# Kernel optimization log

Hardware: AMD Instinct MI355X
Metric: run time of the kernel (lower is better)

The kernel has to match this reference:

```python
import jax, jax.numpy as jnp
import numpy as np

LEVEL = 20            # module default -> 21 max-pool passes, kernels 1x1 .. 41x41 (H,W only)
K_SIG = 10.0          # init arg k: sigmoid weight sharpness
N_POOL = LEVEL + 1    # len(max_pool)
DENOM = N_POOL + 1    # torch: level = len(max_pool) + 1 = 22


def _edge3d(mask):
    # Equivalent to F.conv3d(mask, filt, padding=1) > 0 where filt is the
    # in-plane Laplacian: center 1, 4 H/W-neighbors -0.25, zeros elsewhere.
    p = jnp.pad(mask, ((0, 0), (0, 0), (0, 0), (1, 1), (1, 1)))
    lap = mask - 0.25 * (p[..., :-2, 1:-1] + p[..., 2:, 1:-1]
                         + p[..., 1:-1, :-2] + p[..., 1:-1, 2:])
    return (lap > 0).astype(jnp.float32)


def _mp3(x):
    # stride-1 3x3 max pool over H,W with same padding (pads with -inf like torch MaxPool)
    return jax.lax.reduce_window(x, -jnp.inf, jax.lax.max,
                                 (1, 1, 1, 3, 3), (1, 1, 1, 1, 1),
                                 ((0, 0), (0, 0), (0, 0), (1, 1), (1, 1)))


def _cal_dist(mask):
    edge = _edge3d(mask)  # [B,1,D,H,W] binary
    # maxpool with window (2k+1)x(2k+1) on a binary map == k cascaded 3x3 dilations,
    # so sum_{k=0}^{LEVEL} maxpool_{2k+1}(edge) is computed incrementally.
    def body(i, carry):
        e, acc = carry
        return (_mp3(e), acc + e)
    _, acc = jax.lax.fori_loop(0, N_POOL, body, (edge, jnp.zeros_like(edge)))
    return (DENOM - acc) / DENOM


def setup_inputs() -> dict:
    key = jax.random.key(0)
    k1, k2 = jax.random.split(key)
    outputs = jax.random.uniform(k1, (2, 1, 64, 256, 256), dtype=jnp.float32)
    masks = jax.random.randint(k2, (2, 1, 64, 256, 256), 0, 2, dtype=jnp.int32)
    return {"outputs": outputs, "masks": masks}


def reference(outputs, masks):
    eps = 1e-6
    m = masks.astype(jnp.float32)
    dist = _cal_dist(m)
    weight = jax.lax.stop_gradient(2.0 / (1.0 + jnp.exp(K_SIG * dist)))
    b = outputs.shape[0]
    ow = (outputs.astype(jnp.float32) * weight).reshape(b, -1)
    mw = (m * weight).reshape(b, -1)
    intersect = jnp.sum(ow * m.reshape(b, -1), axis=1)
    input_area = jnp.sum(ow, axis=1)
    target_area = jnp.sum(mw, axis=1)
    batch_loss = 1.0 - 2.0 * intersect / (input_area + target_area + 2.0 * eps)
    batch_loss = jnp.where(target_area == 0, 0.0, batch_loss)
    return batch_loss.mean()
```

## Files before the change

### kernel.cpp

```cpp
#include <hip/hip_runtime.h>
#include <stdint.h>

typedef unsigned long long u64;

#define SLICES 128
#define WPS 1024
#define TOTAL_WORDS (SLICES * WPS)
#define NBLK3 512


__global__ __launch_bounds__(256) void k_pack(const int* __restrict__ masks,
                                              u64* __restrict__ mbits) {
    const int lane = threadIdx.x & 63;
    const int wave = (blockIdx.x * 256 + threadIdx.x) >> 6;
    const int nwaves = (gridDim.x * 256) >> 6;
    #pragma unroll 4
    for (int w = wave; w < TOTAL_WORDS; w += nwaves) {
        int v = masks[(size_t)w * 64 + lane];
        u64 bal = __ballot(v != 0);
        if (lane == 0) mbits[w] = bal;
    }
}

__global__ __launch_bounds__(256) void k_dilate(const u64* __restrict__ mbits,
                                                u64* __restrict__ planes) {
    __shared__ u64 rows[256][5];
    __shared__ u64 tmp[256][5];

    const int t = threadIdx.x;
    const int slice = blockIdx.x;
    const u64* mb = mbits + (size_t)slice * WPS;

    u64 m[4];
    #pragma unroll
    for (int j = 0; j < 4; ++j) { m[j] = mb[t * 4 + j]; rows[t][j] = m[j]; }
    __syncthreads();

    u64 c[4];
    {
        u64 up[4], dn[4];
        #pragma unroll
        for (int j = 0; j < 4; ++j) {
            up[j] = (t > 0)   ? rows[t - 1][j] : 0ull;
            dn[j] = (t < 255) ? rows[t + 1][j] : 0ull;
        }
        #pragma unroll
        for (int j = 0; j < 4; ++j) {
            u64 lf = (m[j] << 1) | (j > 0 ? (m[j - 1] >> 63) : 0ull);
            u64 rt = (m[j] >> 1) | (j < 3 ? (m[j + 1] << 63) : 0ull);
            c[j] = m[j] & ~(up[j] & dn[j] & lf & rt);
        }
    }

    u64 p[5][4];
    #pragma unroll
    for (int pl = 0; pl < 5; ++pl)
        #pragma unroll
        for (int j = 0; j < 4; ++j) p[pl][j] = 0ull;

    __syncthreads();

    for (int k = 1; k <= 20; ++k) {
        u64 h[4];
        #pragma unroll
        for (int j = 0; j < 4; ++j) {
            u64 lf = (c[j] << 1) | (j > 0 ? (c[j - 1] >> 63) : 0ull);
            u64 rt = (c[j] >> 1) | (j < 3 ? (c[j + 1] << 63) : 0ull);
            h[j] = c[j] | lf | rt;
            tmp[t][j] = h[j];
        }
        __syncthreads();
        #pragma unroll
        for (int j = 0; j < 4; ++j) {
            u64 u_ = (t > 0)   ? tmp[t - 1][j] : 0ull;
            u64 d_ = (t < 255) ? tmp[t + 1][j] : 0ull;
            u64 n = h[j] | u_ | d_;
            u64 nw = n & ~c[j];
            c[j] = n;
            #pragma unroll
            for (int pl = 0; pl < 5; ++pl)
                if ((k >> pl) & 1) p[pl][j] |= nw;
        }
        int done = ((c[0] & c[1] & c[2] & c[3]) == 0xFFFFFFFFFFFFFFFFull) ? 1 : 0;
        if (__syncthreads_and(done)) break;
    }

    #pragma unroll
    for (int j = 0; j < 4; ++j) {
        u64 u_ = ~c[j];
        p[0][j] |= u_; p[2][j] |= u_; p[4][j] |= u_;
    }

    #pragma unroll
    for (int pl = 0; pl < 5; ++pl)
        #pragma unroll
        for (int j = 0; j < 4; ++j)
            planes[(size_t)pl * TOTAL_WORDS + (size_t)slice * WPS + t * 4 + j] = p[pl][j];
}

__global__ __launch_bounds__(256) void k_reduce(const float* __restrict__ outputs,
                                               const u64* __restrict__ mbits,
                                               const u64* __restrict__ planes,
                                               float* __restrict__ partials) {
    __shared__ float wtab[22];
    __shared__ float red[4][6];
    const int t = threadIdx.x;
    if (t < 22) wtab[t] = 2.0f / (1.0f + __expf(10.0f * (float)(t + 1) * (1.0f / 22.0f)));
    __syncthreads();

    const int tid = blockIdx.x * 256 + t;
    float s[2][3];
    #pragma unroll
    for (int b = 0; b < 2; ++b) { s[b][0] = s[b][1] = s[b][2] = 0.0f; }

    #pragma unroll
    for (int b = 0; b < 2; ++b) {
        for (int i = 0; i < 8; ++i) {
            int pix4 = b * 1048576 + i * 131072 + tid;
            int pix = pix4 * 4;
            float4 o4 = ((const float4*)outputs)[pix4];
            float ov[4] = {o4.x, o4.y, o4.z, o4.w};
            int widx = pix >> 6;
            int sh = pix & 63;
            u64 mw = mbits[widx];
            u64 p0 = planes[widx];
            u64 p1 = planes[TOTAL_WORDS + widx];
            u64 p2 = planes[2 * TOTAL_WORDS + widx];
            u64 p3 = planes[3 * TOTAL_WORDS + widx];
            u64 p4 = planes[4 * TOTAL_WORDS + widx];
            #pragma unroll
            for (int q = 0; q < 4; ++q) {
                int s2 = sh + q;
                int d0 = (int)((p0 >> s2) & 1ull)
                       | ((int)((p1 >> s2) & 1ull) << 1)
                       | ((int)((p2 >> s2) & 1ull) << 2)
                       | ((int)((p3 >> s2) & 1ull) << 3)
                       | ((int)((p4 >> s2) & 1ull) << 4);
                float w = wtab[d0];
                float ow = ov[q] * w;
                s[b][0] += ow;
                if ((mw >> s2) & 1ull) { s[b][1] += w; s[b][2] += ow; }
            }
        }
    }

    #pragma unroll
    for (int b = 0; b < 2; ++b)
        #pragma unroll
        for (int k = 0; k < 3; ++k) {
            float v = s[b][k];
            #pragma unroll
            for (int off = 32; off > 0; off >>= 1) v += __shfl_down(v, off);
            s[b][k] = v;
        }
    const int lane = t & 63, wv = t >> 6;
    if (lane == 0) {
        #pragma unroll
        for (int b = 0; b < 2; ++b)
            #pragma unroll
            for (int k = 0; k < 3; ++k) red[wv][b * 3 + k] = s[b][k];
    }
    __syncthreads();
    if (t < 6) {
        float v = red[0][t] + red[1][t] + red[2][t] + red[3][t];
        partials[blockIdx.x * 6 + t] = v;
    }
}

__global__ __launch_bounds__(64) void k_fin(const float* __restrict__ partials,
                                            float* __restrict__ out) {
    const int lane = threadIdx.x;
    float s[6] = {0, 0, 0, 0, 0, 0};
    for (int i = lane; i < NBLK3; i += 64)
        #pragma unroll
        for (int k = 0; k < 6; ++k) s[k] += partials[i * 6 + k];
    #pragma unroll
    for (int k = 0; k < 6; ++k) {
        float v = s[k];
        #pragma unroll
        for (int off = 32; off > 0; off >>= 1) v += __shfl_down(v, off);
        s[k] = v;
    }
    if (lane == 0) {
        float loss = 0.0f;
        #pragma unroll
        for (int b = 0; b < 2; ++b) {
            float A = s[b * 3 + 0];
            float T = s[b * 3 + 1];
            float I = s[b * 3 + 2];
            float l = (T == 0.0f) ? 0.0f : (1.0f - 2.0f * I / (A + T + 2e-6f));
            loss += l;
        }
        out[0] = 0.5f * loss;
    }
}

extern "C" void kernel_launch(void* const* d_in, const int* in_sizes, int n_in,
                              void* d_out, int out_size, void* d_ws, size_t ws_size,
                              hipStream_t stream) {
    const float* outputs = (const float*)d_in[0];
    const int* masks = (const int*)d_in[1];
    float* out = (float*)d_out;

    u64* mbits = (u64*)d_ws;
    u64* planes = mbits + TOTAL_WORDS;
    float* partials = (float*)((char*)d_ws + (size_t)6 * TOTAL_WORDS * 8);

    k_pack<<<1024, 256, 0, stream>>>(masks, mbits);
    k_dilate<<<SLICES, 256, 0, stream>>>(mbits, planes);
    k_reduce<<<NBLK3, 256, 0, stream>>>(outputs, mbits, planes, partials);
    k_fin<<<1, 64, 0, stream>>>(partials, out);
}
```

Baseline: 115.1 us.

## Fuse mask bit-packing into dilation kernel and double reduce grid size

Removes the separate pack kernel: each dilation block now reads its slice's int mask directly with int4 loads and builds the 64-bit words in registers, saving a launch and a global round trip for the packed bits. The reduce kernel grid doubles, with each thread handling half as many pixel groups. The risk is that only 128 blocks now read the full 33 MB of masks, each thread striding 1 KB rows, so the mask read bandwidth may be poor compared to the 1024-block pack kernel.

```diff
diff --git a/kernel.cpp b/kernel.cpp
--- a/kernel.cpp
+++ b/kernel.cpp
@@ -6,34 +6,35 @@
 #define SLICES 128
 #define WPS 1024
 #define TOTAL_WORDS (SLICES * WPS)
-#define NBLK3 512
-
-
-__global__ __launch_bounds__(256) void k_pack(const int* __restrict__ masks,
-                                              u64* __restrict__ mbits) {
-    const int lane = threadIdx.x & 63;
-    const int wave = (blockIdx.x * 256 + threadIdx.x) >> 6;
-    const int nwaves = (gridDim.x * 256) >> 6;
-    #pragma unroll 4
-    for (int w = wave; w < TOTAL_WORDS; w += nwaves) {
-        int v = masks[(size_t)w * 64 + lane];
-        u64 bal = __ballot(v != 0);
-        if (lane == 0) mbits[w] = bal;
-    }
-}
-
-__global__ __launch_bounds__(256) void k_dilate(const u64* __restrict__ mbits,
-                                                u64* __restrict__ planes) {
+#define NBLK3 1024
+
+
+__global__ __launch_bounds__(256) void k_packdilate(const int* __restrict__ masks,
+                                                    u64* __restrict__ mbits,
+                                                    u64* __restrict__ planes) {
     __shared__ u64 rows[256][5];
     __shared__ u64 tmp[256][5];
 
     const int t = threadIdx.x;
     const int slice = blockIdx.x;
-    const u64* mb = mbits + (size_t)slice * WPS;
 
     u64 m[4];
-    #pragma unroll
-    for (int j = 0; j < 4; ++j) { m[j] = mb[t * 4 + j]; rows[t][j] = m[j]; }
+    const int4* src = (const int4*)(masks + (size_t)slice * 65536 + t * 256);
+    #pragma unroll
+    for (int j = 0; j < 4; ++j) {
+        u64 w = 0ull;
+        #pragma unroll
+        for (int g = 0; g < 16; ++g) {
+            int4 v = src[j * 16 + g];
+            w |= (u64)(v.x != 0) << (g * 4 + 0);
+            w |= (u64)(v.y != 0) << (g * 4 + 1);
+            w |= (u64)(v.z != 0) << (g * 4 + 2);
+            w |= (u64)(v.w != 0) << (g * 4 + 3);
+        }
+        m[j] = w;
+        rows[t][j] = w;
+        mbits[(size_t)slice * WPS + t * 4 + j] = w;
+    }
     __syncthreads();
 
     u64 c[4];
@@ -58,7 +59,6 @@
         #pragma unroll
         for (int j = 0; j < 4; ++j) p[pl][j] = 0ull;
 
-    __syncthreads();
 
     for (int k = 1; k <= 20; ++k) {
         u64 h[4];
@@ -115,8 +115,8 @@
 
     #pragma unroll
     for (int b = 0; b < 2; ++b) {
-        for (int i = 0; i < 8; ++i) {
-            int pix4 = b * 1048576 + i * 131072 + tid;
+        for (int i = 0; i < 4; ++i) {
+            int pix4 = b * 1048576 + i * 262144 + tid;
             int pix = pix4 * 4;
             float4 o4 = ((const float4*)outputs)[pix4];
             float ov[4] = {o4.x, o4.y, o4.z, o4.w};
@@ -206,8 +206,7 @@
     u64* planes = mbits + TOTAL_WORDS;
     float* partials = (float*)((char*)d_ws + (size_t)6 * TOTAL_WORDS * 8);
 
-    k_pack<<<1024, 256, 0, stream>>>(masks, mbits);
-    k_dilate<<<SLICES, 256, 0, stream>>>(mbits, planes);
+    k_packdilate<<<SLICES, 256, 0, stream>>>(masks, mbits, planes);
     k_reduce<<<NBLK3, 256, 0, stream>>>(outputs, mbits, planes, partials);
     k_fin<<<1, 64, 0, stream>>>(partials, out);
 }
```

Result: no change. 113.2 us, median of 2 (-1.7%).
